# Performance work log

Measured on AMD Instinct MI355X. Metric: run time of the kernel, lower is better.

The kernel has to match this reference:

```python
import jax, jax.numpy as jnp
import numpy as np

SIGMA_S = 1.0
SIGMA_R = 0.1
FR = int(np.ceil(3 * SIGMA_S))          # 3
K_SIZE = 2 * FR + 1                     # 7
B, C, H, W = 8, 3, 512, 512


def matlab_style_gauss2d(shape, sigma):
    m, n = [(ss - 1.0) / 2.0 for ss in shape]
    y, x = np.ogrid[-m:m + 1, -n:n + 1]
    h = np.exp(-(x * x + y * y) / (2.0 * sigma * sigma))
    h[h < np.finfo(h.dtype).eps * h.max()] = 0
    s = h.sum()
    if s != 0:
        h /= s
    return h.astype(np.float32)


GAUSS = matlab_style_gauss2d((K_SIZE, K_SIZE), SIGMA_S)  # [7,7]


def setup_inputs() -> dict:
    key = jax.random.key(0)
    x = jax.random.uniform(key, (B, C, H, W), dtype=jnp.float32)
    return {"input": x}


def reference(input) -> jnp.ndarray:
    # ReflectionPad2d(fr)
    padded = jnp.pad(input, ((0, 0), (0, 0), (FR, FR), (FR, FR)), mode="reflect")
    inv_2sr2 = 1.0 / (2.0 * SIGMA_R * SIGMA_R)
    loss_map = jnp.zeros_like(input)
    for k in range(K_SIZE):
        for l in range(K_SIZE):
            shifted = padded[:, :, k:k + H, l:l + W]            # [B,C,H,W]
            d = input - shifted
            # bilateral range weight * gaussian spatial weight (constant, as in
            # the original which stores weight_map as a raw non-grad tensor)
            w = jax.lax.stop_gradient(
                jnp.exp(-(d * d).sum(1, keepdims=True) * inv_2sr2) * GAUSS[k, l]
            )                                                    # [B,1,H,W]
            loss_map = loss_map + jnp.abs(d) * w
    return loss_map.mean()
```

## Files before the change

### kernel.cpp

```cpp
#include <hip/hip_runtime.h>

#define FR 3
#define KS 7
#define TLX 128
#define TLY 16
#define PPT 4
#define PPX 2
#define HX (TLX + 2*FR)
#define HY (TLY + FR)
#define LSTR 136
#define IMG_H 512
#define IMG_W 512
#define NB 8
#define NC 3
#define GXB (IMG_W / TLX)
#define GYB (IMG_H / TLY)
#define NMAIN (GXB * GYB * NB)
#define RIM_PER_IMG 6108
#define NRIM_THREADS (RIM_PER_IMG * NB)
#define NRIM_BLK ((NRIM_THREADS + 255) / 256)
#define NBLK_A (NMAIN + NRIM_BLK)
#define NPART NBLK_A

#define KSC 8.493218f
#define K2F 72.134752f

constexpr double g1d[KS] = {0.011108996538242306, 0.1353352832366127,
                            0.6065306597126334,   1.0,
                            0.6065306597126334,   0.1353352832366127,
                            0.011108996538242306};
constexpr double SUMG = 1.0 + 2.0 * (0.011108996538242306 + 0.1353352832366127
                                     + 0.6065306597126334);
constexpr double INVN = 1.0 / (SUMG * SUMG);
constexpr double KD   = 8.493218;
constexpr double WPAIR = 2.0 * INVN / KD;

__device__ __forceinline__ int refl(int i, int n) {
    i = (i < 0) ? -i : i;
    return (i >= n) ? (2*n - 2 - i) : i;
}

__global__ __launch_bounds__(256) void blt_fused(const float* __restrict__ in,
                                                 float* __restrict__ partial) {
    __shared__ float sm[NC][HY][LSTR];
    __shared__ float wsum[4];
    const int tid = threadIdx.x;
    float a = 0.0f;

    if (blockIdx.x < NMAIN) {
        const int bid = blockIdx.x;
        const int b   = bid >> 7;
        const int rem = bid & 127;
        const int by  = (rem >> 2) * TLY;
        const int bx  = (rem & 3) * TLX;
        const int tx  = tid & 63;
        const int ty  = tid >> 6;
        const float* base = in + (size_t)b * NC * IMG_H * IMG_W;

        for (int idx = tid; idx < HY * HX; idx += 256) {
            int ly = idx / HX;
            int lx = idx - ly * HX;
            int gy = refl(by + ly - FR, IMG_H);
            int gx = refl(bx + lx - FR, IMG_W);
            #pragma unroll
            for (int c = 0; c < NC; ++c)
                sm[c][ly][lx] = base[(c * IMG_H + gy) * IMG_W + gx] * KSC;
        }
        __syncthreads();

        const int x0 = bx + 2 * tx;
        float glm0[KS], glm1[KS];
        #pragma unroll
        for (int l = 0; l < KS; ++l) {
            glm0[l] = ((unsigned)(x0 + l - FR)     < (unsigned)IMG_W) ? (float)(g1d[l] * WPAIR) : 0.0f;
            glm1[l] = ((unsigned)(x0 + 1 + l - FR) < (unsigned)IMG_W) ? (float)(g1d[l] * WPAIR) : 0.0f;
        }

        const int r0 = ty * PPT;
        float cc0[PPT][PPX], cc1[PPT][PPX], cc2[PPT][PPX];
        float acc0 = 0.0f, acc1 = 0.0f;

        #pragma unroll
        for (int rr = KS - 1; rr >= 0; --rr) {
            float w0[8], w1[8], w2[8];
            #pragma unroll
            for (int j = 0; j < 4; ++j) {
                float2 t0 = *reinterpret_cast<const float2*>(&sm[0][r0 + rr][2 * tx + 2 * j]);
                float2 t1 = *reinterpret_cast<const float2*>(&sm[1][r0 + rr][2 * tx + 2 * j]);
                float2 t2 = *reinterpret_cast<const float2*>(&sm[2][r0 + rr][2 * tx + 2 * j]);
                w0[2*j] = t0.x; w0[2*j+1] = t0.y;
                w1[2*j] = t1.x; w1[2*j+1] = t1.y;
                w2[2*j] = t2.x; w2[2*j+1] = t2.y;
            }
            #pragma unroll
            for (int i = 0; i < PPT; ++i) {
                const int k = rr - i;
                if (k < 0 || k > FR) continue;
                if (k == FR) {
                    cc0[i][0] = w0[3]; cc0[i][1] = w0[4];
                    cc1[i][0] = w1[3]; cc1[i][1] = w1[4];
                    cc2[i][0] = w2[3]; cc2[i][1] = w2[4];
                }
                const int lmax = (k == FR) ? FR : KS;
                const float rw = (by + r0 + i + k >= FR) ? (float)g1d[k] : 0.0f;
                float t0 = 0.0f, t1 = 0.0f;
                #pragma unroll
                for (int l = 0; l < KS; ++l) {
                    if (l >= lmax) continue;
                    {
                        float d0 = cc0[i][0] - w0[l];
                        float d1 = cc1[i][0] - w1[l];
                        float d2 = cc2[i][0] - w2[l];
                        float s = d0 * d0;
                        s = fmaf(d1, d1, s);
                        s = fmaf(d2, d2, s);
                        float e = __builtin_amdgcn_exp2f(-s);
                        float sa = fabsf(d0) + fabsf(d1);
                        sa += fabsf(d2);
                        t0 = fmaf(sa, e * glm0[l], t0);
                    }
                    {
                        float d0 = cc0[i][1] - w0[l + 1];
                        float d1 = cc1[i][1] - w1[l + 1];
                        float d2 = cc2[i][1] - w2[l + 1];
                        float s = d0 * d0;
                        s = fmaf(d1, d1, s);
                        s = fmaf(d2, d2, s);
                        float e = __builtin_amdgcn_exp2f(-s);
                        float sa = fabsf(d0) + fabsf(d1);
                        sa += fabsf(d2);
                        t1 = fmaf(sa, e * glm1[l], t1);
                    }
                }
                acc0 = fmaf(t0, rw, acc0);
                acc1 = fmaf(t1, rw, acc1);
            }
        }
        a = acc0 + acc1;
    } else {
        const int idx = (blockIdx.x - NMAIN) * 256 + tid;
        if (idx < NRIM_THREADS) {
            const int b = idx / RIM_PER_IMG;
            int r = idx - b * RIM_PER_IMG;
            int y, x;
            if (r < 3 * IMG_W) { y = r >> 9; x = r & (IMG_W - 1); }
            else if (r < 6 * IMG_W) { r -= 3 * IMG_W; y = (IMG_H - 3) + (r >> 9); x = r & (IMG_W - 1); }
            else if (r < 6 * IMG_W + 3 * (IMG_H - 6)) { r -= 6 * IMG_W; y = 3 + r / 3; x = r - 3 * (r / 3); }
            else { r -= 6 * IMG_W + 3 * (IMG_H - 6); y = 3 + r / 3; x = (IMG_W - 3) + (r - 3 * (r / 3)); }

            const float* base = in + (size_t)b * NC * IMG_H * IMG_W;
            const float cc0 = base[(0 * IMG_H + y) * IMG_W + x];
            const float cc1 = base[(1 * IMG_H + y) * IMG_W + x];
            const float cc2 = base[(2 * IMG_H + y) * IMG_W + x];

            #pragma unroll
            for (int k = 0; k < KS; ++k) {
                #pragma unroll
                for (int l = 0; l < KS; ++l) {
                    if (k == FR && l == FR) continue;
                    int qy = y + k - FR, qx = x + l - FR;
                    bool oob = ((unsigned)qy >= (unsigned)IMG_H) | ((unsigned)qx >= (unsigned)IMG_W);
                    if (oob) {
                        int ry = refl(qy, IMG_H), rx = refl(qx, IMG_W);
                        float v0 = base[(0 * IMG_H + ry) * IMG_W + rx];
                        float v1 = base[(1 * IMG_H + ry) * IMG_W + rx];
                        float v2 = base[(2 * IMG_H + ry) * IMG_W + rx];
                        float d0 = cc0 - v0, d1 = cc1 - v1, d2 = cc2 - v2;
                        float s = d0 * d0;
                        s = fmaf(d1, d1, s);
                        s = fmaf(d2, d2, s);
                        float e = __builtin_amdgcn_exp2f(-(K2F * s));
                        float sa = fabsf(d0) + fabsf(d1) + fabsf(d2);
                        a = fmaf(sa, e * (float)(g1d[k] * g1d[l] * INVN), a);
                    }
                }
            }
        }
        __syncthreads();
    }

    #pragma unroll
    for (int off = 32; off > 0; off >>= 1)
        a += __shfl_down(a, off, 64);
    if ((tid & 63) == 0) wsum[tid >> 6] = a;
    __syncthreads();
    if (tid == 0)
        partial[blockIdx.x] = wsum[0] + wsum[1] + wsum[2] + wsum[3];
}

__global__ __launch_bounds__(256) void finalize_kernel(const float* __restrict__ partial,
                                                       float* __restrict__ out) {
    __shared__ float wsum[4];
    const int tid = threadIdx.x;
    float a = 0.0f;
    for (int i = tid; i < NPART; i += 256) a += partial[i];
    #pragma unroll
    for (int off = 32; off > 0; off >>= 1)
        a += __shfl_down(a, off, 64);
    if ((tid & 63) == 0) wsum[tid >> 6] = a;
    __syncthreads();
    if (tid == 0)
        out[0] = (wsum[0] + wsum[1] + wsum[2] + wsum[3]) / (float)(NB * NC * IMG_H * IMG_W);
}

extern "C" void kernel_launch(void* const* d_in, const int* in_sizes, int n_in,
                              void* d_out, int out_size, void* d_ws, size_t ws_size,
                              hipStream_t stream) {
    const float* in = (const float*)d_in[0];
    float* out = (float*)d_out;
    float* ws  = (float*)d_ws;

    blt_fused<<<NBLK_A, 256, 0, stream>>>(in, ws);
    finalize_kernel<<<1, 256, 0, stream>>>(ws, out);
}
```

Measured before the change: 94.73 us.

## Pack pixel-pair math into float2 vectors and launch rim blocks first

```diff
diff --git a/kernel.cpp b/kernel.cpp
--- a/kernel.cpp
+++ b/kernel.cpp
@@ -5,7 +5,6 @@
 #define TLX 128
 #define TLY 16
 #define PPT 4
-#define PPX 2
 #define HX (TLX + 2*FR)
 #define HY (TLY + FR)
 #define LSTR 136
@@ -25,6 +24,9 @@
 #define KSC 8.493218f
 #define K2F 72.134752f
 
+typedef float v2f __attribute__((ext_vector_type(2)));
+__device__ __forceinline__ v2f mk2(float a, float b) { v2f r; r.x = a; r.y = b; return r; }
+
 constexpr double g1d[KS] = {0.011108996538242306, 0.1353352832366127,
                             0.6065306597126334,   1.0,
                             0.6065306597126334,   0.1353352832366127,
@@ -47,8 +49,8 @@
     const int tid = threadIdx.x;
     float a = 0.0f;
 
-    if (blockIdx.x < NMAIN) {
-        const int bid = blockIdx.x;
+    if (blockIdx.x >= NRIM_BLK) {
+        const int bid = blockIdx.x - NRIM_BLK;
         const int b   = bid >> 7;
         const int rem = bid & 127;
         const int by  = (rem >> 2) * TLY;
@@ -69,76 +71,74 @@
         __syncthreads();
 
         const int x0 = bx + 2 * tx;
-        float glm0[KS], glm1[KS];
+        v2f glmv[KS];
         #pragma unroll
         for (int l = 0; l < KS; ++l) {
-            glm0[l] = ((unsigned)(x0 + l - FR)     < (unsigned)IMG_W) ? (float)(g1d[l] * WPAIR) : 0.0f;
-            glm1[l] = ((unsigned)(x0 + 1 + l - FR) < (unsigned)IMG_W) ? (float)(g1d[l] * WPAIR) : 0.0f;
+            float m0 = ((unsigned)(x0 + l - FR)     < (unsigned)IMG_W) ? (float)(g1d[l] * WPAIR) : 0.0f;
+            float m1 = ((unsigned)(x0 + 1 + l - FR) < (unsigned)IMG_W) ? (float)(g1d[l] * WPAIR) : 0.0f;
+            glmv[l] = mk2(m0, m1);
         }
 
         const int r0 = ty * PPT;
-        float cc0[PPT][PPX], cc1[PPT][PPX], cc2[PPT][PPX];
-        float acc0 = 0.0f, acc1 = 0.0f;
+        v2f ccv[PPT][NC];
+        v2f acc[PPT];
+        #pragma unroll
+        for (int i = 0; i < PPT; ++i) acc[i] = mk2(0.0f, 0.0f);
 
         #pragma unroll
         for (int rr = KS - 1; rr >= 0; --rr) {
-            float w0[8], w1[8], w2[8];
-            #pragma unroll
-            for (int j = 0; j < 4; ++j) {
-                float2 t0 = *reinterpret_cast<const float2*>(&sm[0][r0 + rr][2 * tx + 2 * j]);
-                float2 t1 = *reinterpret_cast<const float2*>(&sm[1][r0 + rr][2 * tx + 2 * j]);
-                float2 t2 = *reinterpret_cast<const float2*>(&sm[2][r0 + rr][2 * tx + 2 * j]);
-                w0[2*j] = t0.x; w0[2*j+1] = t0.y;
-                w1[2*j] = t1.x; w1[2*j+1] = t1.y;
-                w2[2*j] = t2.x; w2[2*j+1] = t2.y;
+            v2f wp[NC][KS];
+            #pragma unroll
+            for (int c = 0; c < NC; ++c) {
+                v2f p0 = *reinterpret_cast<const v2f*>(&sm[c][r0 + rr][2 * tx + 0]);
+                v2f p1 = *reinterpret_cast<const v2f*>(&sm[c][r0 + rr][2 * tx + 2]);
+                v2f p2 = *reinterpret_cast<const v2f*>(&sm[c][r0 + rr][2 * tx + 4]);
+                v2f p3 = *reinterpret_cast<const v2f*>(&sm[c][r0 + rr][2 * tx + 6]);
+                wp[c][0] = p0;
+                wp[c][1] = mk2(p0.y, p1.x);
+                wp[c][2] = p1;
+                wp[c][3] = mk2(p1.y, p2.x);
+                wp[c][4] = p2;
+                wp[c][5] = mk2(p2.y, p3.x);
+                wp[c][6] = p3;
             }
             #pragma unroll
             for (int i = 0; i < PPT; ++i) {
                 const int k = rr - i;
                 if (k < 0 || k > FR) continue;
                 if (k == FR) {
-                    cc0[i][0] = w0[3]; cc0[i][1] = w0[4];
-                    cc1[i][0] = w1[3]; cc1[i][1] = w1[4];
-                    cc2[i][0] = w2[3]; cc2[i][1] = w2[4];
+                    ccv[i][0] = wp[0][3];
+                    ccv[i][1] = wp[1][3];
+                    ccv[i][2] = wp[2][3];
                 }
                 const int lmax = (k == FR) ? FR : KS;
-                const float rw = (by + r0 + i + k >= FR) ? (float)g1d[k] : 0.0f;
-                float t0 = 0.0f, t1 = 0.0f;
+                const float rw = (by + r0 + rr >= FR) ? (float)g1d[k] : 0.0f;
+                v2f t = mk2(0.0f, 0.0f);
                 #pragma unroll
                 for (int l = 0; l < KS; ++l) {
                     if (l >= lmax) continue;
-                    {
-                        float d0 = cc0[i][0] - w0[l];
-                        float d1 = cc1[i][0] - w1[l];
-                        float d2 = cc2[i][0] - w2[l];
-                        float s = d0 * d0;
-                        s = fmaf(d1, d1, s);
-                        s = fmaf(d2, d2, s);
-                        float e = __builtin_amdgcn_exp2f(-s);
-                        float sa = fabsf(d0) + fabsf(d1);
-                        sa += fabsf(d2);
-                        t0 = fmaf(sa, e * glm0[l], t0);
-                    }
-                    {
-                        float d0 = cc0[i][1] - w0[l + 1];
-                        float d1 = cc1[i][1] - w1[l + 1];
-                        float d2 = cc2[i][1] - w2[l + 1];
-                        float s = d0 * d0;
-                        s = fmaf(d1, d1, s);
-                        s = fmaf(d2, d2, s);
-                        float e = __builtin_amdgcn_exp2f(-s);
-                        float sa = fabsf(d0) + fabsf(d1);
-                        sa += fabsf(d2);
-                        t1 = fmaf(sa, e * glm1[l], t1);
-                    }
+                    v2f d0 = ccv[i][0] - wp[0][l];
+                    v2f d1 = ccv[i][1] - wp[1][l];
+                    v2f d2 = ccv[i][2] - wp[2][l];
+                    v2f s  = d0 * d0;
+                    s = __builtin_elementwise_fma(d1, d1, s);
+                    s = __builtin_elementwise_fma(d2, d2, s);
+                    v2f e;
+                    e.x = __builtin_amdgcn_exp2f(-s.x);
+                    e.y = __builtin_amdgcn_exp2f(-s.y);
+                    float sax = fabsf(d0.x) + fabsf(d1.x);
+                    sax += fabsf(d2.x);
+                    float say = fabsf(d0.y) + fabsf(d1.y);
+                    say += fabsf(d2.y);
+                    t = __builtin_elementwise_fma(mk2(sax, say), e * glmv[l], t);
                 }
-                acc0 = fmaf(t0, rw, acc0);
-                acc1 = fmaf(t1, rw, acc1);
+                acc[i] = __builtin_elementwise_fma(t, mk2(rw, rw), acc[i]);
             }
         }
-        a = acc0 + acc1;
+        v2f av = (acc[0] + acc[1]) + (acc[2] + acc[3]);
+        a = av.x + av.y;
     } else {
-        const int idx = (blockIdx.x - NMAIN) * 256 + tid;
+        const int idx = blockIdx.x * 256 + tid;
         if (idx < NRIM_THREADS) {
             const int b = idx / RIM_PER_IMG;
             int r = idx - b * RIM_PER_IMG;
```

Measured after the change: 94.40 us. No clear change (-0.3%).

## Use interleaved float4 channel tile, smaller tiles, and rim blocks first

Applied to the files above, without the earlier changes.

```diff
diff --git a/kernel.cpp b/kernel.cpp
--- a/kernel.cpp
+++ b/kernel.cpp
@@ -2,13 +2,11 @@
 
 #define FR 3
 #define KS 7
-#define TLX 128
-#define TLY 16
-#define PPT 4
-#define PPX 2
+#define TLX 64
+#define TLY 8
+#define PPT 2
 #define HX (TLX + 2*FR)
 #define HY (TLY + FR)
-#define LSTR 136
 #define IMG_H 512
 #define IMG_W 512
 #define NB 8
@@ -42,17 +40,17 @@
 
 __global__ __launch_bounds__(256) void blt_fused(const float* __restrict__ in,
                                                  float* __restrict__ partial) {
-    __shared__ float sm[NC][HY][LSTR];
+    __shared__ float4 smv[HY * HX];
     __shared__ float wsum[4];
     const int tid = threadIdx.x;
     float a = 0.0f;
 
-    if (blockIdx.x < NMAIN) {
-        const int bid = blockIdx.x;
-        const int b   = bid >> 7;
-        const int rem = bid & 127;
-        const int by  = (rem >> 2) * TLY;
-        const int bx  = (rem & 3) * TLX;
+    if (blockIdx.x >= NRIM_BLK) {
+        const int bid = blockIdx.x - NRIM_BLK;
+        const int b   = bid >> 9;
+        const int rem = bid & 511;
+        const int by  = (rem >> 3) * TLY;
+        const int bx  = (rem & 7) * TLX;
         const int tx  = tid & 63;
         const int ty  = tid >> 6;
         const float* base = in + (size_t)b * NC * IMG_H * IMG_W;
@@ -62,83 +60,58 @@
             int lx = idx - ly * HX;
             int gy = refl(by + ly - FR, IMG_H);
             int gx = refl(bx + lx - FR, IMG_W);
-            #pragma unroll
-            for (int c = 0; c < NC; ++c)
-                sm[c][ly][lx] = base[(c * IMG_H + gy) * IMG_W + gx] * KSC;
+            float4 p;
+            p.x = base[(0 * IMG_H + gy) * IMG_W + gx] * KSC;
+            p.y = base[(1 * IMG_H + gy) * IMG_W + gx] * KSC;
+            p.z = base[(2 * IMG_H + gy) * IMG_W + gx] * KSC;
+            p.w = 0.0f;
+            smv[idx] = p;
         }
         __syncthreads();
 
-        const int x0 = bx + 2 * tx;
-        float glm0[KS], glm1[KS];
+        const int x0 = bx + tx;
+        float glm[KS];
         #pragma unroll
-        for (int l = 0; l < KS; ++l) {
-            glm0[l] = ((unsigned)(x0 + l - FR)     < (unsigned)IMG_W) ? (float)(g1d[l] * WPAIR) : 0.0f;
-            glm1[l] = ((unsigned)(x0 + 1 + l - FR) < (unsigned)IMG_W) ? (float)(g1d[l] * WPAIR) : 0.0f;
-        }
+        for (int l = 0; l < KS; ++l)
+            glm[l] = ((unsigned)(x0 + l - FR) < (unsigned)IMG_W) ? (float)(g1d[l] * WPAIR) : 0.0f;
 
         const int r0 = ty * PPT;
-        float cc0[PPT][PPX], cc1[PPT][PPX], cc2[PPT][PPX];
+        const float4* wbase = &smv[r0 * HX + tx];
+
         float acc0 = 0.0f, acc1 = 0.0f;
-
         #pragma unroll
-        for (int rr = KS - 1; rr >= 0; --rr) {
-            float w0[8], w1[8], w2[8];
+        for (int i = 0; i < PPT; ++i) {
+            const float4 c = wbase[(i + FR) * HX + FR];
+            float accp = 0.0f;
             #pragma unroll
-            for (int j = 0; j < 4; ++j) {
-                float2 t0 = *reinterpret_cast<const float2*>(&sm[0][r0 + rr][2 * tx + 2 * j]);
-                float2 t1 = *reinterpret_cast<const float2*>(&sm[1][r0 + rr][2 * tx + 2 * j]);
-                float2 t2 = *reinterpret_cast<const float2*>(&sm[2][r0 + rr][2 * tx + 2 * j]);
-                w0[2*j] = t0.x; w0[2*j+1] = t0.y;
-                w1[2*j] = t1.x; w1[2*j+1] = t1.y;
-                w2[2*j] = t2.x; w2[2*j+1] = t2.y;
-            }
-            #pragma unroll
-            for (int i = 0; i < PPT; ++i) {
-                const int k = rr - i;
-                if (k < 0 || k > FR) continue;
-                if (k == FR) {
-                    cc0[i][0] = w0[3]; cc0[i][1] = w0[4];
-                    cc1[i][0] = w1[3]; cc1[i][1] = w1[4];
-                    cc2[i][0] = w2[3]; cc2[i][1] = w2[4];
-                }
+            for (int k = 0; k <= FR; ++k) {
                 const int lmax = (k == FR) ? FR : KS;
                 const float rw = (by + r0 + i + k >= FR) ? (float)g1d[k] : 0.0f;
-                float t0 = 0.0f, t1 = 0.0f;
+                float t = 0.0f;
                 #pragma unroll
                 for (int l = 0; l < KS; ++l) {
                     if (l >= lmax) continue;
-                    {
-                        float d0 = cc0[i][0] - w0[l];
-                        float d1 = cc1[i][0] - w1[l];
-                        float d2 = cc2[i][0] - w2[l];
-                        float s = d0 * d0;
-                        s = fmaf(d1, d1, s);
-                        s = fmaf(d2, d2, s);
-                        float e = __builtin_amdgcn_exp2f(-s);
-                        float sa = fabsf(d0) + fabsf(d1);
-                        sa += fabsf(d2);
-                        t0 = fmaf(sa, e * glm0[l], t0);
-                    }
-                    {
-                        float d0 = cc0[i][1] - w0[l + 1];
-                        float d1 = cc1[i][1] - w1[l + 1];
-                        float d2 = cc2[i][1] - w2[l + 1];
-                        float s = d0 * d0;
-                        s = fmaf(d1, d1, s);
-                        s = fmaf(d2, d2, s);
-                        float e = __builtin_amdgcn_exp2f(-s);
-                        float sa = fabsf(d0) + fabsf(d1);
-                        sa += fabsf(d2);
-                        t1 = fmaf(sa, e * glm1[l], t1);
-                    }
+                    const float4 v = wbase[(i + k) * HX + l];
+                    float d0 = c.x - v.x;
+                    float d1 = c.y - v.y;
+                    float d2 = c.z - v.z;
+                    float d3 = c.w - v.w;
+                    float s = d0 * d0;
+                    s = fmaf(d1, d1, s);
+                    s = fmaf(d2, d2, s);
+                    s = fmaf(d3, d3, s);
+                    float e = __builtin_amdgcn_exp2f(-s);
+                    float sa = fabsf(d0) + fabsf(d1);
+                    sa += fabsf(d2);
+                    t = fmaf(sa, e * glm[l], t);
                 }
-                acc0 = fmaf(t0, rw, acc0);
-                acc1 = fmaf(t1, rw, acc1);
+                accp = fmaf(t, rw, accp);
             }
+            if (i == 0) acc0 = accp; else acc1 = accp;
         }
         a = acc0 + acc1;
     } else {
-        const int idx = (blockIdx.x - NMAIN) * 256 + tid;
+        const int idx = blockIdx.x * 256 + tid;
         if (idx < NRIM_THREADS) {
             const int b = idx / RIM_PER_IMG;
             int r = idx - b * RIM_PER_IMG;
```

Result: no change. 96.40 us (+1.8%).

## Shrink tiles to 64x16, add interior fast path, schedule rim blocks first

Applied to the files above, without the earlier changes.

```diff
diff --git a/kernel.cpp b/kernel.cpp
--- a/kernel.cpp
+++ b/kernel.cpp
@@ -2,13 +2,11 @@
 
 #define FR 3
 #define KS 7
-#define TLX 128
+#define TLX 64
 #define TLY 16
-#define PPT 4
-#define PPX 2
 #define HX (TLX + 2*FR)
 #define HY (TLY + FR)
-#define LSTR 136
+#define LSTR 72
 #define IMG_H 512
 #define IMG_W 512
 #define NB 8
@@ -47,14 +45,16 @@
     const int tid = threadIdx.x;
     float a = 0.0f;
 
-    if (blockIdx.x < NMAIN) {
-        const int bid = blockIdx.x;
-        const int b   = bid >> 7;
-        const int rem = bid & 127;
-        const int by  = (rem >> 2) * TLY;
-        const int bx  = (rem & 3) * TLX;
-        const int tx  = tid & 63;
-        const int ty  = tid >> 6;
+    if (blockIdx.x >= NRIM_BLK) {
+        const int bid = blockIdx.x - NRIM_BLK;
+        const int b   = bid >> 8;
+        const int rem = bid & 255;
+        const int byi = rem >> 3;
+        const int bxi = rem & 7;
+        const int by  = byi * TLY;
+        const int bx  = bxi * TLX;
+        const int tx  = tid & 31;
+        const int ty  = tid >> 5;
         const float* base = in + (size_t)b * NC * IMG_H * IMG_W;
 
         for (int idx = tid; idx < HY * HX; idx += 256) {
@@ -68,77 +68,118 @@
         }
         __syncthreads();
 
-        const int x0 = bx + 2 * tx;
-        float glm0[KS], glm1[KS];
-        #pragma unroll
-        for (int l = 0; l < KS; ++l) {
-            glm0[l] = ((unsigned)(x0 + l - FR)     < (unsigned)IMG_W) ? (float)(g1d[l] * WPAIR) : 0.0f;
-            glm1[l] = ((unsigned)(x0 + 1 + l - FR) < (unsigned)IMG_W) ? (float)(g1d[l] * WPAIR) : 0.0f;
+        const int r0 = ty * 2;
+        float cc[NC][2][2];
+
+        if ((bxi != 0) & (bxi != GXB - 1) & (byi != 0)) {
+            #pragma unroll
+            for (int rr = 4; rr >= 0; --rr) {
+                float w[NC][8];
+                #pragma unroll
+                for (int c = 0; c < NC; ++c) {
+                    const float2* rp = reinterpret_cast<const float2*>(&sm[c][r0 + rr][2 * tx]);
+                    float2 p0 = rp[0], p1 = rp[1], p2 = rp[2], p3 = rp[3];
+                    w[c][0] = p0.x; w[c][1] = p0.y; w[c][2] = p1.x; w[c][3] = p1.y;
+                    w[c][4] = p2.x; w[c][5] = p2.y; w[c][6] = p3.x; w[c][7] = p3.y;
+                }
+                #pragma unroll
+                for (int i = 0; i < 2; ++i) {
+                    const int k = rr - i;
+                    if (k < 0 || k > FR) continue;
+                    if (k == FR) {
+                        #pragma unroll
+                        for (int c = 0; c < NC; ++c) {
+                            cc[c][i][0] = w[c][3];
+                            cc[c][i][1] = w[c][4];
+                        }
+                    }
+                    const int lmax = (k == FR) ? FR : KS;
+                    #pragma unroll
+                    for (int j = 0; j < 2; ++j) {
+                        #pragma unroll
+                        for (int l = 0; l < KS; ++l) {
+                            if (l >= lmax) continue;
+                            float d0 = cc[0][i][j] - w[0][l + j];
+                            float d1 = cc[1][i][j] - w[1][l + j];
+                            float d2 = cc[2][i][j] - w[2][l + j];
+                            float s = d0 * d0;
+                            s = fmaf(d1, d1, s);
+                            s = fmaf(d2, d2, s);
+                            float e = __builtin_amdgcn_exp2f(-s);
+                            float sa = fabsf(d0) + fabsf(d1);
+                            sa += fabsf(d2);
+                            a = fmaf(sa, e * (float)(g1d[k] * g1d[l] * WPAIR), a);
+                        }
+                    }
+                }
+            }
+        } else {
+            const int x0 = bx + 2 * tx;
+            float glm0[KS], glm1[KS];
+            #pragma unroll
+            for (int l = 0; l < KS; ++l) {
+                glm0[l] = ((unsigned)(x0 + l - FR)     < (unsigned)IMG_W) ? (float)(g1d[l] * WPAIR) : 0.0f;
+                glm1[l] = ((unsigned)(x0 + 1 + l - FR) < (unsigned)IMG_W) ? (float)(g1d[l] * WPAIR) : 0.0f;
+            }
+            #pragma unroll
+            for (int rr = 4; rr >= 0; --rr) {
+                float w[NC][8];
+                #pragma unroll
+                for (int c = 0; c < NC; ++c) {
+                    const float2* rp = reinterpret_cast<const float2*>(&sm[c][r0 + rr][2 * tx]);
+                    float2 p0 = rp[0], p1 = rp[1], p2 = rp[2], p3 = rp[3];
+                    w[c][0] = p0.x; w[c][1] = p0.y; w[c][2] = p1.x; w[c][3] = p1.y;
+                    w[c][4] = p2.x; w[c][5] = p2.y; w[c][6] = p3.x; w[c][7] = p3.y;
+                }
+                #pragma unroll
+                for (int i = 0; i < 2; ++i) {
+                    const int k = rr - i;
+                    if (k < 0 || k > FR) continue;
+                    if (k == FR) {
+                        #pragma unroll
+                        for (int c = 0; c < NC; ++c) {
+                            cc[c][i][0] = w[c][3];
+                            cc[c][i][1] = w[c][4];
+                        }
+                    }
+                    const int lmax = (k == FR) ? FR : KS;
+                    const float rw = (by + r0 + rr >= FR) ? (float)g1d[k] : 0.0f;
+                    float t0 = 0.0f, t1 = 0.0f;
+                    #pragma unroll
+                    for (int l = 0; l < KS; ++l) {
+                        if (l >= lmax) continue;
+                        {
+                            float d0 = cc[0][i][0] - w[0][l];
+                            float d1 = cc[1][i][0] - w[1][l];
+                            float d2 = cc[2][i][0] - w[2][l];
+                            float s = d0 * d0;
+                            s = fmaf(d1, d1, s);
+                            s = fmaf(d2, d2, s);
+                            float e = __builtin_amdgcn_exp2f(-s);
+                            float sa = fabsf(d0) + fabsf(d1);
+                            sa += fabsf(d2);
+                            t0 = fmaf(sa, e * glm0[l], t0);
+                        }
+                        {
+                            float d0 = cc[0][i][1] - w[0][l + 1];
+                            float d1 = cc[1][i][1] - w[1][l + 1];
+                            float d2 = cc[2][i][1] - w[2][l + 1];
+                            float s = d0 * d0;
+                            s = fmaf(d1, d1, s);
+                            s = fmaf(d2, d2, s);
+                            float e = __builtin_amdgcn_exp2f(-s);
+                            float sa = fabsf(d0) + fabsf(d1);
+                            sa += fabsf(d2);
+                            t1 = fmaf(sa, e * glm1[l], t1);
+                        }
+                    }
+                    a = fmaf(t0, rw, a);
+                    a = fmaf(t1, rw, a);
+                }
+            }
         }
-
-        const int r0 = ty * PPT;
-        float cc0[PPT][PPX], cc1[PPT][PPX], cc2[PPT][PPX];
-        float acc0 = 0.0f, acc1 = 0.0f;
-
-        #pragma unroll
-        for (int rr = KS - 1; rr >= 0; --rr) {
-            float w0[8], w1[8], w2[8];
-            #pragma unroll
-            for (int j = 0; j < 4; ++j) {
-                float2 t0 = *reinterpret_cast<const float2*>(&sm[0][r0 + rr][2 * tx + 2 * j]);
-                float2 t1 = *reinterpret_cast<const float2*>(&sm[1][r0 + rr][2 * tx + 2 * j]);
-                float2 t2 = *reinterpret_cast<const float2*>(&sm[2][r0 + rr][2 * tx + 2 * j]);
-                w0[2*j] = t0.x; w0[2*j+1] = t0.y;
-                w1[2*j] = t1.x; w1[2*j+1] = t1.y;
-                w2[2*j] = t2.x; w2[2*j+1] = t2.y;
-            }
-            #pragma unroll
-            for (int i = 0; i < PPT; ++i) {
-                const int k = rr - i;
-                if (k < 0 || k > FR) continue;
-                if (k == FR) {
-                    cc0[i][0] = w0[3]; cc0[i][1] = w0[4];
-                    cc1[i][0] = w1[3]; cc1[i][1] = w1[4];
-                    cc2[i][0] = w2[3]; cc2[i][1] = w2[4];
-                }
-                const int lmax = (k == FR) ? FR : KS;
-                const float rw = (by + r0 + i + k >= FR) ? (float)g1d[k] : 0.0f;
-                float t0 = 0.0f, t1 = 0.0f;
-                #pragma unroll
-                for (int l = 0; l < KS; ++l) {
-                    if (l >= lmax) continue;
-                    {
-                        float d0 = cc0[i][0] - w0[l];
-                        float d1 = cc1[i][0] - w1[l];
-                        float d2 = cc2[i][0] - w2[l];
-                        float s = d0 * d0;
-                        s = fmaf(d1, d1, s);
-                        s = fmaf(d2, d2, s);
-                        float e = __builtin_amdgcn_exp2f(-s);
-                        float sa = fabsf(d0) + fabsf(d1);
-                        sa += fabsf(d2);
-                        t0 = fmaf(sa, e * glm0[l], t0);
-                    }
-                    {
-                        float d0 = cc0[i][1] - w0[l + 1];
-                        float d1 = cc1[i][1] - w1[l + 1];
-                        float d2 = cc2[i][1] - w2[l + 1];
-                        float s = d0 * d0;
-                        s = fmaf(d1, d1, s);
-                        s = fmaf(d2, d2, s);
-                        float e = __builtin_amdgcn_exp2f(-s);
-                        float sa = fabsf(d0) + fabsf(d1);
-                        sa += fabsf(d2);
-                        t1 = fmaf(sa, e * glm1[l], t1);
-                    }
-                }
-                acc0 = fmaf(t0, rw, acc0);
-                acc1 = fmaf(t1, rw, acc1);
-            }
-        }
-        a = acc0 + acc1;
     } else {
-        const int idx = (blockIdx.x - NMAIN) * 256 + tid;
+        const int idx = blockIdx.x * 256 + tid;
         if (idx < NRIM_THREADS) {
             const int b = idx / RIM_PER_IMG;
             int r = idx - b * RIM_PER_IMG;
```

New measurement: 90.95 us, median of 2. 4.0% less time.
